# Kernel tuning notes

Hardware: AMD Instinct MI355X
Metric: run time of the kernel (lower is better)

The kernel has to match this reference:

```python
import jax, jax.numpy as jnp
import numpy as np

# (dy, dx) offsets corresponding to the single -1 entries of kernels 1..8
# delta1 rows: (0,0),(0,1),(0,2),(1,2); delta2 = spatial flip: (2,2),(2,1),(2,0),(1,0)
OFFSETS = [(-1, -1), (-1, 0), (-1, 1), (0, 1), (1, 1), (1, 0), (1, -1), (0, -1)]
NUM_LAYER = 9
EPS = 1e-12


def _shift(x, dy, dx):
    # zero-padded shift: out[y, x] = in[y + dy, x + dx]; dilation = shifts[0] = 1
    b, c, h, w = x.shape
    p = jnp.pad(x, ((0, 0), (0, 0), (1, 1), (1, 1)))
    return jax.lax.dynamic_slice(p, (0, 0, 1 + dy, 1 + dx), (b, c, h, w))


def _l2norm(v, axis):
    # matches torch.nn.functional.normalize: v / max(||v||, eps)
    n = jnp.sqrt(jnp.sum(v * v, axis=axis, keepdims=True))
    return v / jnp.maximum(n, EPS)


def setup_inputs() -> dict:
    key = jax.random.key(0)
    k1, k2, k3, k4 = jax.random.split(key, 4)
    B, C, H, W = 4, 256, 96, 96
    cen = jax.random.normal(k1, (B, C, H, W), dtype=jnp.float32)
    scale = 1.0 / np.sqrt(C)
    # grouped 1x1 convs (groups=9): per-group (C x C) weight matrices
    W1 = jax.random.normal(k2, (NUM_LAYER, C, C), dtype=jnp.float32) * scale
    W2 = jax.random.normal(k3, (C, C), dtype=jnp.float32) * scale
    W3 = jax.random.normal(k4, (NUM_LAYER, C, C), dtype=jnp.float32) * scale
    return {"cen": cen, "W1": W1, "W2": W2, "W3": W3}


def reference(cen, W1, W2, W3):
    b, c, h, w = cen.shape
    # Extract_layer: 8 fixed depthwise 3x3 convs (each = negated shift) + identity
    surrounds = jnp.stack(
        [-_shift(cen, dy, dx) for dy, dx in OFFSETS] + [cen], axis=1
    )  # (b, 9, c, h, w)
    # Analyze_layer: grouped 1x1 convs = per-group matmuls
    out1 = jnp.einsum("gij,bgjhw->bgihw", W1, surrounds)
    out2 = jnp.einsum("ij,bjhw->bihw", W2, cen)[:, None]  # (b, 1, c, h, w)
    out3 = jnp.einsum("gij,bgjhw->bgihw", W3, surrounds)
    out1 = _l2norm(out1, axis=2)
    out2 = _l2norm(out2, axis=2)
    out3 = _l2norm(out3, axis=2)
    # softmax over a size-1 axis (dim=2 after mean+keepdim) -> identically 1.0
    att = jax.nn.softmax(
        jnp.mean(out1 * out2, axis=2, keepdims=True), axis=2
    )  # (b, 9, 1, h, w)
    out = jnp.sum(att * out3, axis=1)  # (b, c, h, w)
    return out + cen
```

## Files before the change

kernel.cpp:

```cpp
#include <hip/hip_runtime.h>
#include <stdint.h>

#define BB 4
#define CC 256
#define HH 96
#define WW 96
#define HP 98
#define CP 264
#define XT 32
#define YT 2
#define XE 34

typedef __bf16 bf16x8 __attribute__((ext_vector_type(8)));
typedef __bf16 bf16x16 __attribute__((ext_vector_type(16)));
typedef float f32x4 __attribute__((ext_vector_type(4)));
typedef float f32x16 __attribute__((ext_vector_type(16)));

__device__ __forceinline__ uint16_t f2bf(float f) {
    uint32_t u = __float_as_uint(f);
    u += 0x7FFFu + ((u >> 16) & 1u);
    return (uint16_t)(u >> 16);
}

__global__ void zero_halo(uint16_t* __restrict__ cenT) {
    int idx = blockIdx.x * 256 + threadIdx.x;
    if (idx >= 1552 * 33) return;
    int p = idx / 33, q = idx - p * 33;
    int b = p / 388, s = p - b * 388;
    int y, x;
    if (s < 98)      { y = 0;       x = s; }
    else if (s < 196){ y = 97;      x = s - 98; }
    else if (s < 292){ x = 0;       y = s - 196 + 1; }
    else             { x = 97;      y = s - 292 + 1; }
    size_t o = (((size_t)b * HP + y) * HP + x) * CP + q * 8;
    *(uint4*)(cenT + o) = make_uint4(0u, 0u, 0u, 0u);
}

__global__ void transpose_cen(const float* __restrict__ cen, uint16_t* __restrict__ cenT) {
    const int y = blockIdx.x, b = blockIdx.y, ch = blockIdx.z, tid = threadIdx.x;
    __shared__ uint16_t ldsX[128 * 100];

    #pragma unroll
    for (int i = 0; i < 12; ++i) {
        int f = i * 256 + tid;
        int c = f / 24, xq = f % 24;
        float4 v = *(const float4*)(cen + ((((size_t)b * CC + ch * 128 + c) * HH + y) * WW + xq * 4));
        uint2 pk;
        pk.x = (uint32_t)f2bf(v.x) | ((uint32_t)f2bf(v.y) << 16);
        pk.y = (uint32_t)f2bf(v.z) | ((uint32_t)f2bf(v.w) << 16);
        *(uint2*)(&ldsX[c * 100 + xq * 4]) = pk;
    }
    __syncthreads();
    #pragma unroll
    for (int i = 0; i < 6; ++i) {
        int t = i * 256 + tid;
        int x = t % 96, cq = t / 96;
        uint32_t w0, w1, w2, w3;
        w0 = (uint32_t)ldsX[(cq * 8 + 0) * 100 + x] | ((uint32_t)ldsX[(cq * 8 + 1) * 100 + x] << 16);
        w1 = (uint32_t)ldsX[(cq * 8 + 2) * 100 + x] | ((uint32_t)ldsX[(cq * 8 + 3) * 100 + x] << 16);
        w2 = (uint32_t)ldsX[(cq * 8 + 4) * 100 + x] | ((uint32_t)ldsX[(cq * 8 + 5) * 100 + x] << 16);
        w3 = (uint32_t)ldsX[(cq * 8 + 6) * 100 + x] | ((uint32_t)ldsX[(cq * 8 + 7) * 100 + x] << 16);
        size_t o = (((size_t)b * HP + (y + 1)) * HP + (x + 1)) * CP + ch * 128 + cq * 8;
        *(uint4*)(cenT + o) = make_uint4(w0, w1, w2, w3);
    }
}

__global__ void cvt_w3(const float* __restrict__ W3, uint16_t* __restrict__ W3bf) {
    int e = (blockIdx.x * 256 + threadIdx.x) * 4;
    int g = e >> 16, n = (e >> 8) & 255, k = e & 255;
    float4 v = *(const float4*)(W3 + e);
    uint2 pk;
    pk.x = (uint32_t)f2bf(v.x) | ((uint32_t)f2bf(v.y) << 16);
    pk.y = (uint32_t)f2bf(v.z) | ((uint32_t)f2bf(v.w) << 16);
    size_t o = (size_t)(((g * 8 + (n >> 5)) * 16 + (k >> 4)) * 512)
             + (n & 31) * 16 + ((k >> 3) & 1) * 8 + (k & 7);
    *(uint2*)(W3bf + o) = pk;
}

__global__ __launch_bounds__(256, 2)
void ecm_main(const float* __restrict__ cen, const uint16_t* __restrict__ cenT,
              const uint16_t* __restrict__ W3bf, float* __restrict__ out) {
    const int tid = threadIdx.x;
    const int wv = tid >> 6, lane = tid & 63, col = lane & 31, kh = lane >> 5;
    const int x0 = blockIdx.x * XT, y0 = blockIdx.y * YT, b = blockIdx.z;

    __shared__ __align__(16) uint16_t ldsA[YT * XE * CP];
    __shared__ __align__(16) float ldsP[2][64][4];

    const int dgOrd[9] = {0, 1, 2, 7, 8, 3, 6, 5, 4};

    const uint16_t* wbA = W3bf + (size_t)(2 * wv) * (16 * 512) + col * 16 + kh * 8;
    bf16x16 finA0 = {}, finA1 = {}, finB0 = {}, finB1 = {};

    #pragma unroll 1
    for (int idx = 0; idx < 9; ++idx) {
        const int g = dgOrd[idx], dg = idx / 3, dx = idx % 3 - 1;

        if (idx % 3 == 0) {
            for (int r = 0; r < YT; ++r) {
                const uint4* gs = (const uint4*)(cenT + (((size_t)b * HP + (y0 + dg + r)) * HP + x0) * CP);
                uint4* ls = (uint4*)(ldsA + r * XE * CP);
                for (int c = tid; c < XE * CP / 8; c += 256) ls[c] = gs[c];
            }
            __syncthreads();
        }

        const uint16_t* wgA = wbA + (size_t)g * 65536;
        const uint16_t* wgB = wgA + 16 * 512;
        const int a0 = (col + dx + 1) * CP + kh * 8;
        const int a1 = a0 + XE * CP;

        f32x16 aA0 = {}, aA1 = {}, aB0 = {}, aB1 = {};

        bf16x8 qA[3], qB[3];
        #pragma unroll
        for (int i = 0; i < 3; ++i) {
            qA[i] = *(const bf16x8*)(wgA + i * 512);
            qB[i] = *(const bf16x8*)(wgB + i * 512);
        }
        bf16x8 b0 = *(const bf16x8*)(ldsA + a0);
        bf16x8 b1 = *(const bf16x8*)(ldsA + a1);

        #pragma unroll
        for (int ks = 0; ks < 16; ++ks) {
            bf16x8 wa = qA[ks % 3], wb = qB[ks % 3];
            if (ks + 3 < 16) {
                qA[ks % 3] = *(const bf16x8*)(wgA + (ks + 3) * 512);
                qB[ks % 3] = *(const bf16x8*)(wgB + (ks + 3) * 512);
            }
            bf16x8 n0 = b0, n1 = b1;
            if (ks + 1 < 16) {
                n0 = *(const bf16x8*)(ldsA + a0 + (ks + 1) * 16);
                n1 = *(const bf16x8*)(ldsA + a1 + (ks + 1) * 16);
            }
            __builtin_amdgcn_s_setprio(1);
            aA0 = __builtin_amdgcn_mfma_f32_32x32x16_bf16(wa, b0, aA0, 0, 0, 0);
            aB0 = __builtin_amdgcn_mfma_f32_32x32x16_bf16(wb, b0, aB0, 0, 0, 0);
            aA1 = __builtin_amdgcn_mfma_f32_32x32x16_bf16(wa, b1, aA1, 0, 0, 0);
            aB1 = __builtin_amdgcn_mfma_f32_32x32x16_bf16(wb, b1, aB1, 0, 0, 0);
            __builtin_amdgcn_s_setprio(0);
            b0 = n0; b1 = n1;
        }

        float s0 = 0.f, s1 = 0.f;
        #pragma unroll
        for (int r = 0; r < 16; ++r) {
            s0 += aA0[r] * aA0[r] + aB0[r] * aB0[r];
            s1 += aA1[r] * aA1[r] + aB1[r] * aB1[r];
        }
        s0 += __shfl_xor(s0, 32, 64);
        s1 += __shfl_xor(s1, 32, 64);
        if (kh == 0) { ldsP[idx & 1][col][wv] = s0; ldsP[idx & 1][32 + col][wv] = s1; }
        __syncthreads();

        f32x4 pa = *(const f32x4*)&ldsP[idx & 1][col][0];
        f32x4 qa = *(const f32x4*)&ldsP[idx & 1][32 + col][0];
        float n0 = pa[0] + pa[1] + pa[2] + pa[3];
        float n1 = qa[0] + qa[1] + qa[2] + qa[3];
        const float sgn = (g == 8) ? 1.f : -1.f;
        float sc0 = sgn / fmaxf(sqrtf(n0), 1e-12f);
        float sc1 = sgn / fmaxf(sqrtf(n1), 1e-12f);
        #pragma unroll
        for (int r = 0; r < 16; ++r) {
            finA0[r] = (__bf16)((float)finA0[r] + aA0[r] * sc0);
            finB0[r] = (__bf16)((float)finB0[r] + aB0[r] * sc0);
            finA1[r] = (__bf16)((float)finA1[r] + aA1[r] * sc1);
            finB1[r] = (__bf16)((float)finB1[r] + aB1[r] * sc1);
        }
    }

    #pragma unroll
    for (int r = 0; r < 16; ++r) {
        int chA = wv * 64 + (r & 3) + 8 * (r >> 2) + 4 * kh;
        size_t oA0 = (((size_t)b * CC + chA) * HH + y0) * WW + (x0 + col);
        size_t oA1 = oA0 + WW;
        out[oA0] = (float)finA0[r] + cen[oA0];
        out[oA1] = (float)finA1[r] + cen[oA1];
        size_t oB0 = oA0 + (size_t)32 * HH * WW;
        size_t oB1 = oB0 + WW;
        out[oB0] = (float)finB0[r] + cen[oB0];
        out[oB1] = (float)finB1[r] + cen[oB1];
    }
}

extern "C" void kernel_launch(void* const* d_in, const int* in_sizes, int n_in,
                              void* d_out, int out_size, void* d_ws, size_t ws_size,
                              hipStream_t stream) {
    const float* cen = (const float*)d_in[0];
    const float* W3 = (const float*)d_in[3];
    float* out = (float*)d_out;

    uint16_t* cenT = (uint16_t*)d_ws;
    const size_t cenT_elems = (size_t)BB * HP * HP * CP;
    uint16_t* W3bf = cenT + cenT_elems;

    zero_halo<<<201, 256, 0, stream>>>(cenT);
    transpose_cen<<<dim3(HH, BB, 2), 256, 0, stream>>>(cen, cenT);
    cvt_w3<<<576, 256, 0, stream>>>(W3, W3bf);
    ecm_main<<<dim3(3, 48, 4), 256, 0, stream>>>(cen, cenT, W3bf, out);
}
```

Before: 174.7 us.

## Stream W3 fragments through per-wave LDS double buffer via global_load_lds

```diff
diff --git a/kernel.cpp b/kernel.cpp
--- a/kernel.cpp
+++ b/kernel.cpp
@@ -20,6 +20,12 @@
     uint32_t u = __float_as_uint(f);
     u += 0x7FFFu + ((u >> 16) & 1u);
     return (uint16_t)(u >> 16);
+}
+
+__device__ __forceinline__ void gll16(const uint16_t* g, uint16_t* l) {
+    __builtin_amdgcn_global_load_lds(
+        (const __attribute__((address_space(1))) uint32_t*)g,
+        (__attribute__((address_space(3))) uint32_t*)l, 16, 0, 0);
 }
 
 __global__ void zero_halo(uint16_t* __restrict__ cenT) {
@@ -73,7 +79,7 @@
     pk.x = (uint32_t)f2bf(v.x) | ((uint32_t)f2bf(v.y) << 16);
     pk.y = (uint32_t)f2bf(v.z) | ((uint32_t)f2bf(v.w) << 16);
     size_t o = (size_t)(((g * 8 + (n >> 5)) * 16 + (k >> 4)) * 512)
-             + (n & 31) * 16 + ((k >> 3) & 1) * 8 + (k & 7);
+             + ((k >> 3) & 1) * 256 + (n & 31) * 8 + (k & 7);
     *(uint2*)(W3bf + o) = pk;
 }
 
@@ -85,11 +91,13 @@
     const int x0 = blockIdx.x * XT, y0 = blockIdx.y * YT, b = blockIdx.z;
 
     __shared__ __align__(16) uint16_t ldsA[YT * XE * CP];
+    __shared__ __align__(16) uint16_t ldsW[4 * 4096];
     __shared__ __align__(16) float ldsP[2][64][4];
 
     const int dgOrd[9] = {0, 1, 2, 7, 8, 3, 6, 5, 4};
 
-    const uint16_t* wbA = W3bf + (size_t)(2 * wv) * (16 * 512) + col * 16 + kh * 8;
+    const int fo = lane * 8;
+    uint16_t* wds = ldsW + wv * 4096;
     bf16x16 finA0 = {}, finA1 = {}, finB0 = {}, finB1 = {};
 
     #pragma unroll 1
@@ -105,41 +113,49 @@
             __syncthreads();
         }
 
-        const uint16_t* wgA = wbA + (size_t)g * 65536;
-        const uint16_t* wgB = wgA + 16 * 512;
+        const uint16_t* wsrc = W3bf + (size_t)g * 65536 + fo;
         const int a0 = (col + dx + 1) * CP + kh * 8;
         const int a1 = a0 + XE * CP;
 
+        #pragma unroll
+        for (int q = 0; q < 2; ++q)
+            #pragma unroll
+            for (int j = 0; j < 4; ++j) {
+                int t = 2 * wv + (j & 1), ksa = 2 * q + (j >> 1);
+                gll16(wsrc + ((size_t)t * 16 + ksa) * 512, wds + q * 2048 + j * 512);
+            }
+
         f32x16 aA0 = {}, aA1 = {}, aB0 = {}, aB1 = {};
 
-        bf16x8 qA[3], qB[3];
-        #pragma unroll
-        for (int i = 0; i < 3; ++i) {
-            qA[i] = *(const bf16x8*)(wgA + i * 512);
-            qB[i] = *(const bf16x8*)(wgB + i * 512);
-        }
-        bf16x8 b0 = *(const bf16x8*)(ldsA + a0);
-        bf16x8 b1 = *(const bf16x8*)(ldsA + a1);
-
-        #pragma unroll
-        for (int ks = 0; ks < 16; ++ks) {
-            bf16x8 wa = qA[ks % 3], wb = qB[ks % 3];
-            if (ks + 3 < 16) {
-                qA[ks % 3] = *(const bf16x8*)(wgA + (ks + 3) * 512);
-                qB[ks % 3] = *(const bf16x8*)(wgB + (ks + 3) * 512);
-            }
-            bf16x8 n0 = b0, n1 = b1;
-            if (ks + 1 < 16) {
-                n0 = *(const bf16x8*)(ldsA + a0 + (ks + 1) * 16);
-                n1 = *(const bf16x8*)(ldsA + a1 + (ks + 1) * 16);
-            }
-            __builtin_amdgcn_s_setprio(1);
-            aA0 = __builtin_amdgcn_mfma_f32_32x32x16_bf16(wa, b0, aA0, 0, 0, 0);
-            aB0 = __builtin_amdgcn_mfma_f32_32x32x16_bf16(wb, b0, aB0, 0, 0, 0);
-            aA1 = __builtin_amdgcn_mfma_f32_32x32x16_bf16(wa, b1, aA1, 0, 0, 0);
-            aB1 = __builtin_amdgcn_mfma_f32_32x32x16_bf16(wb, b1, aB1, 0, 0, 0);
-            __builtin_amdgcn_s_setprio(0);
-            b0 = n0; b1 = n1;
+        #pragma unroll
+        for (int p = 0; p < 8; ++p) {
+            if (p < 7) asm volatile("s_waitcnt vmcnt(4)" ::: "memory");
+            else       asm volatile("s_waitcnt vmcnt(0)" ::: "memory");
+            __builtin_amdgcn_sched_barrier(0);
+
+            const uint16_t* wbuf = wds + (p & 1) * 2048;
+            #pragma unroll
+            for (int s = 0; s < 2; ++s) {
+                const int ks = 2 * p + s;
+                bf16x8 wa = *(const bf16x8*)(wbuf + (s * 2 + 0) * 512 + fo);
+                bf16x8 wb = *(const bf16x8*)(wbuf + (s * 2 + 1) * 512 + fo);
+                bf16x8 b0 = *(const bf16x8*)(ldsA + a0 + ks * 16);
+                bf16x8 b1 = *(const bf16x8*)(ldsA + a1 + ks * 16);
+                aA0 = __builtin_amdgcn_mfma_f32_32x32x16_bf16(wa, b0, aA0, 0, 0, 0);
+                aB0 = __builtin_amdgcn_mfma_f32_32x32x16_bf16(wb, b0, aB0, 0, 0, 0);
+                aA1 = __builtin_amdgcn_mfma_f32_32x32x16_bf16(wa, b1, aA1, 0, 0, 0);
+                aB1 = __builtin_amdgcn_mfma_f32_32x32x16_bf16(wb, b1, aB1, 0, 0, 0);
+            }
+
+            __builtin_amdgcn_sched_barrier(0);
+            if (p < 6) {
+                #pragma unroll
+                for (int j = 0; j < 4; ++j) {
+                    int t = 2 * wv + (j & 1), ksa = 2 * (p + 2) + (j >> 1);
+                    gll16(wsrc + ((size_t)t * 16 + ksa) * 512,
+                          wds + (p & 1) * 2048 + j * 512);
+                }
+            }
         }
 
         float s0 = 0.f, s1 = 0.f;
```

New measurement: 190.4 us. 9.0% more time.
